# Kernel optimization log

Hardware: AMD Instinct MI355X
Metric: run time of the kernel (lower is better)

Reference implementation:

```python
import jax, jax.numpy as jnp
import numpy as np

N = 50000
E = 1600000
F_IN = 4
F_OUT = 32
PERIODS = 12


def setup_inputs() -> dict:
    key = jax.random.key(0)
    ks = jax.random.split(key, 18)
    s_in = 1.0 / np.sqrt(F_IN)
    s_cat = 1.0 / np.sqrt(2 * F_OUT)
    s_out = 1.0 / np.sqrt(F_OUT)
    inp = {
        'x': jax.random.normal(ks[0], (N, F_IN, PERIODS), dtype=jnp.float32),
        'edge_index': jax.random.randint(ks[1], (2, E), 0, N, dtype=jnp.int32),
        'attention': jax.random.uniform(ks[2], (PERIODS,), dtype=jnp.float32),
        # GRU update gate z: GCNConv weight/bias + Linear(2*F_OUT -> F_OUT)
        'Wz': jax.random.normal(ks[3], (F_IN, F_OUT), jnp.float32) * s_in,
        'bz': jnp.zeros((F_OUT,), jnp.float32),
        'Lz': jax.random.normal(ks[4], (2 * F_OUT, F_OUT), jnp.float32) * s_cat,
        'lz': jnp.zeros((F_OUT,), jnp.float32),
        # reset gate r
        'Wr': jax.random.normal(ks[5], (F_IN, F_OUT), jnp.float32) * s_in,
        'br': jnp.zeros((F_OUT,), jnp.float32),
        'Lr': jax.random.normal(ks[6], (2 * F_OUT, F_OUT), jnp.float32) * s_cat,
        'lr': jnp.zeros((F_OUT,), jnp.float32),
        # candidate h
        'Wh': jax.random.normal(ks[7], (F_IN, F_OUT), jnp.float32) * s_in,
        'bh': jnp.zeros((F_OUT,), jnp.float32),
        'Lh': jax.random.normal(ks[8], (2 * F_OUT, F_OUT), jnp.float32) * s_cat,
        'lh': jnp.zeros((F_OUT,), jnp.float32),
        # outer Linear(32 -> periods)
        'Wo': jax.random.normal(ks[9], (F_OUT, PERIODS), jnp.float32) * s_out,
        'bo': jnp.zeros((PERIODS,), jnp.float32),
    }
    return inp


def reference(x, edge_index, attention, Wz, bz, Lz, lz, Wr, br, Lr, lr, Wh, bh, Lh, lh, Wo, bo):
    n = x.shape[0]
    # gcn_norm: add self loops, symmetric D^-1/2 (A+I) D^-1/2
    loop = jnp.arange(n, dtype=edge_index.dtype)
    row = jnp.concatenate([edge_index[0], loop])  # source
    col = jnp.concatenate([edge_index[1], loop])  # target
    w = jnp.ones(row.shape[0], dtype=x.dtype)
    deg = jax.ops.segment_sum(w, col, num_segments=n)
    dinv = jnp.where(deg > 0, jax.lax.rsqrt(deg), 0.0)
    norm = dinv[row] * dinv[col]  # [E+N]

    def conv(xt, W, b):
        h = xt @ W                                   # [N, F_OUT]
        msg = h[row] * norm[:, None]                 # gather + scale
        return jax.ops.segment_sum(msg, col, num_segments=n) + b

    H0 = jnp.zeros((n, F_OUT), dtype=x.dtype)  # A3TGCN passes H=None each period

    def tgcn(xt):
        Z = jax.nn.sigmoid(jnp.concatenate([conv(xt, Wz, bz), H0], axis=1) @ Lz + lz)
        R = jax.nn.sigmoid(jnp.concatenate([conv(xt, Wr, br), H0], axis=1) @ Lr + lr)
        Ht = jnp.tanh(jnp.concatenate([conv(xt, Wh, bh), H0 * R], axis=1) @ Lh + lh)
        return Z * H0 + (1.0 - Z) * Ht

    Hs = jax.vmap(tgcn)(jnp.moveaxis(x, 2, 0))       # [T, N, F_OUT]
    probs = jax.nn.softmax(attention)
    H = jnp.einsum('tnc,t->nc', Hs, probs)           # attention-weighted sum over periods
    return jax.nn.relu(H) @ Wo + bo                  # [N, PERIODS]
```

## Files before the change

kernel.cpp:

```cpp
#include <hip/hip_runtime.h>
#include <hip/hip_fp16.h>
#include <math.h>

#define CHUNK 4096
#define CAPG  5120
#define GNODES 21

union U2H { uint2 u; __half2 h[2]; };

__global__ void k_pre(const float* __restrict__ Wz, const float* __restrict__ Lz, const float* __restrict__ lz,
                      const float* __restrict__ Wh, const float* __restrict__ Lh, const float* __restrict__ lh,
                      const float* __restrict__ bz, const float* __restrict__ bh,
                      const float* __restrict__ att,
                      float* __restrict__ AzT, float* __restrict__ AhT,
                      float* __restrict__ bzp, float* __restrict__ bhp, float* __restrict__ probs,
                      int* __restrict__ gcur) {
  int t = threadIdx.x;
  gcur[t] = 0;
  if (t < 128) {
    int f = t >> 2, k = t & 3;
    float s = 0.f, s2 = 0.f;
    for (int j = 0; j < 32; ++j) {
      s  = fmaf(Wz[k * 32 + j], Lz[j * 32 + f], s);
      s2 = fmaf(Wh[k * 32 + j], Lh[j * 32 + f], s2);
    }
    AzT[t] = s; AhT[t] = s2;
  }
  if (t >= 128 && t < 160) {
    int f = t - 128;
    float s = lz[f], s2 = lh[f];
    for (int j = 0; j < 32; ++j) {
      s  = fmaf(bz[j], Lz[j * 32 + f], s);
      s2 = fmaf(bh[j], Lh[j * 32 + f], s2);
    }
    bzp[f] = s; bhp[f] = s2;
  }
  if (t == 160) {
    float m = att[0];
    for (int i = 1; i < 12; ++i) m = fmaxf(m, att[i]);
    float e[12]; float s = 0.f;
    for (int i = 0; i < 12; ++i) { e[i] = __expf(att[i] - m); s += e[i]; }
    for (int i = 0; i < 12; ++i) probs[i] = e[i] / s;
  }
}

__global__ __launch_bounds__(512) void k_part(const int* __restrict__ row, const int* __restrict__ col,
                                              int E, int nbkt,
                                              int* __restrict__ gcur, unsigned* __restrict__ part) {
  __shared__ unsigned spak[CHUNK];
  __shared__ unsigned short sboth[CHUNK];
  __shared__ int hist[512], sscan[512], scur[512], gbase[512];
  int t = threadIdx.x;
  int base = blockIdx.x * CHUNK;
  int cnt = E - base; if (cnt > CHUNK) cnt = CHUNK;
  hist[t] = 0;
  __syncthreads();
  for (int i = t; i < cnt; i += 512) {
    int c = col[base + i];
    sboth[i] = (unsigned short)c;
    atomicAdd(&hist[c >> 7], 1);
  }
  __syncthreads();
  int v = hist[t];
  sscan[t] = v;
  __syncthreads();
  for (int off = 1; off < 512; off <<= 1) {
    int a = (t >= off) ? sscan[t - off] : 0;
    __syncthreads();
    sscan[t] += a;
    __syncthreads();
  }
  int excl = sscan[t] - v;
  gbase[t] = (v > 0) ? atomicAdd(&gcur[t], v) : 0;
  scur[t] = 0;
  __syncthreads();
  sscan[t] = excl;
  __syncthreads();
  for (int i = t; i < cnt; i += 512) {
    int c = (int)sboth[i];
    int b = c >> 7;
    int pos = atomicAdd(&scur[b], 1);
    spak[sscan[b] + pos] = ((unsigned)row[base + i] << 7) | (unsigned)(c & 127);
  }
  __syncthreads();
  int wave = t >> 6, lane = t & 63;
  for (int b = wave; b < nbkt; b += 8) {
    int len = hist[b], gb = gbase[b], src = sscan[b];
    int lim = CAPG - gb; if (lim > len) lim = len;
    unsigned* dst = part + (size_t)b * CAPG + gb;
    for (int j = lane; j < lim; j += 64) dst[j] = spak[src + j];
  }
}

__global__ __launch_bounds__(512) void k_sort(const unsigned* __restrict__ part, const int* __restrict__ gcur,
                                              const float4* __restrict__ x4,
                                              int* __restrict__ csr, int2* __restrict__ rng,
                                              float* __restrict__ dinv, uint2* __restrict__ xh2, int n) {
  __shared__ unsigned sedge[CAPG];
  __shared__ int hist[128], soff[128], scur2[128];
  __shared__ float sdi[128];
  int b = blockIdx.x, t = threadIdx.x;
  int cnt = gcur[b]; if (cnt > CAPG) cnt = CAPG;
  const unsigned* src = part + (size_t)b * CAPG;
  if (t < 128) hist[t] = 0;
  __syncthreads();
  for (int i = t; i < cnt; i += 512) {
    unsigned e = src[i];
    sedge[i] = e;
    atomicAdd(&hist[e & 127u], 1);
  }
  __syncthreads();
  int v = 0;
  if (t < 128) { v = hist[t]; soff[t] = v; }
  __syncthreads();
  for (int off = 1; off < 128; off <<= 1) {
    int a = 0;
    if (t < 128 && t >= off) a = soff[t - off];
    __syncthreads();
    if (t < 128) soff[t] += a;
    __syncthreads();
  }
  int base = b * CAPG;
  if (t < 128) {
    int excl = soff[t] - v;
    int node = b * 128 + t;
    float di = rsqrtf((float)(v + 1));
    sdi[t] = di;
    if (node < n) {
      rng[node] = make_int2(base + excl, base + excl + v);
      dinv[node] = di;
    }
    soff[t] = excl;
    scur2[t] = 0;
  }
  __syncthreads();
  for (int i = t; i < cnt; i += 512) {
    unsigned e = sedge[i];
    int lc = (int)(e & 127u);
    int pos = atomicAdd(&scur2[lc], 1);
    csr[base + soff[lc] + pos] = (int)(e >> 7);
  }
  int gb = b * 1536;
  for (int j = t; j < 1536; j += 512) {
    int gi = gb + j;
    if (gi < n * 12) {
      float4 f = x4[gi];
      float d = sdi[j / 12];
      __half2 h0 = __floats2half2_rn(d * f.x, d * f.y);
      __half2 h1 = __floats2half2_rn(d * f.z, d * f.w);
      uint2 u; u.x = *(unsigned*)&h0; u.y = *(unsigned*)&h1;
      xh2[gi] = u;
    }
  }
}

__global__ __launch_bounds__(256) void k_gather(const int* __restrict__ csr, const int2* __restrict__ rng,
                                                const float* __restrict__ dinv, const uint2* __restrict__ xh2,
                                                float4* __restrict__ Y4, int n) {
  int t = threadIdx.x;
  int grp = t / 12, c = t - grp * 12;
  if (grp >= GNODES) return;
  int node = blockIdx.x * GNODES + grp;
  if (node >= n) return;
  U2H s; s.u = xh2[(size_t)node * 12 + c];
  float2 f0 = __half22float2(s.h[0]), f1 = __half22float2(s.h[1]);
  float a0 = f0.x, a1 = f0.y, a2 = f1.x, a3 = f1.y;
  int2 r = rng[node];
  int e = r.x, end = r.y;
#define ACC4(V) { \
    float2 g0 = __half22float2(V.h[0]), g1 = __half22float2(V.h[1]); \
    a0 += g0.x; a1 += g0.y; a2 += g1.x; a3 += g1.y; }
  for (; e + 8 <= end; e += 8) {
    int r0 = csr[e],     r1 = csr[e + 1], r2 = csr[e + 2], r3 = csr[e + 3];
    int r4 = csr[e + 4], r5 = csr[e + 5], r6 = csr[e + 6], r7 = csr[e + 7];
    U2H v0, v1, v2, v3, v4, v5, v6, v7;
    v0.u = xh2[(size_t)r0 * 12 + c];
    v1.u = xh2[(size_t)r1 * 12 + c];
    v2.u = xh2[(size_t)r2 * 12 + c];
    v3.u = xh2[(size_t)r3 * 12 + c];
    v4.u = xh2[(size_t)r4 * 12 + c];
    v5.u = xh2[(size_t)r5 * 12 + c];
    v6.u = xh2[(size_t)r6 * 12 + c];
    v7.u = xh2[(size_t)r7 * 12 + c];
    ACC4(v0) ACC4(v1) ACC4(v2) ACC4(v3) ACC4(v4) ACC4(v5) ACC4(v6) ACC4(v7)
  }
  for (; e < end; ++e) {
    int r0 = csr[e];
    U2H v0; v0.u = xh2[(size_t)r0 * 12 + c];
    ACC4(v0)
  }
#undef ACC4
  float di = dinv[node];
  Y4[(size_t)node * 12 + c] = make_float4(a0 * di, a1 * di, a2 * di, a3 * di);
}

__global__ __launch_bounds__(256) void k_dense(
    const float4* __restrict__ Y4,
    const float* __restrict__ AzT, const float* __restrict__ AhT,
    const float* __restrict__ bzp, const float* __restrict__ bhp,
    const float* __restrict__ probs,
    const float* __restrict__ Wo, const float* __restrict__ bo,
    float* __restrict__ out, int n) {
  __shared__ float4 sAz4[32], sAh4[32];
  __shared__ float sbzp[32], sbhp[32], sprobs[12], sbo[12];
  __shared__ float sWo[384];
  __shared__ float4 sY4[96];
  __shared__ float sH[8 * 33];

  int t = threadIdx.x;
  int nb = blockIdx.x * 8;

  if (t < 32) {
    sAz4[t] = ((const float4*)AzT)[t];
    sAh4[t] = ((const float4*)AhT)[t];
    sbzp[t] = bzp[t];
    sbhp[t] = bhp[t];
  }
  if (t >= 32 && t < 44) { sprobs[t - 32] = probs[t - 32]; sbo[t - 32] = bo[t - 32]; }
  for (int i = t; i < 384; i += 256) sWo[i] = Wo[i];
  if (t < 96) {
    int gi = nb * 12 + t;
    if (gi < n * 12) sY4[t] = Y4[gi];
  }
  __syncthreads();

  int ln = t >> 5, f = t & 31;
  float4 az = sAz4[f], ah = sAh4[f];
  float bzf = sbzp[f], bhf = sbhp[f];
  const float* y = (const float*)sY4 + ln * 48;
  float Hf = 0.f;
#pragma unroll
  for (int tt = 0; tt < 12; ++tt) {
    float y0 = y[tt], y1 = y[12 + tt], y2 = y[24 + tt], y3 = y[36 + tt];
    float za = fmaf(az.x, y0, fmaf(az.y, y1, fmaf(az.z, y2, fmaf(az.w, y3, bzf))));
    float ha = fmaf(ah.x, y0, fmaf(ah.y, y1, fmaf(ah.z, y2, fmaf(ah.w, y3, bhf))));
    float ez = __expf(za);
    float ax = fabsf(ha);
    float e2 = __expf(-2.f * ax);
    float g = (1.f - e2) / ((1.f + ez) * (1.f + e2));
    Hf = fmaf(sprobs[tt], copysignf(g, ha), Hf);
  }
  sH[ln * 33 + f] = fmaxf(Hf, 0.f);
  __syncthreads();

  if (t < 96) {
    int ln2 = t / 12, p = t - ln2 * 12;
    int node2 = nb + ln2;
    if (node2 < n) {
      float acc = sbo[p];
      const float* h = &sH[ln2 * 33];
      const float* wv = &sWo[p];
#pragma unroll
      for (int f2 = 0; f2 < 32; ++f2) acc = fmaf(h[f2], wv[f2 * 12], acc);
      out[node2 * 12 + p] = acc;
    }
  }
}

extern "C" void kernel_launch(void* const* d_in, const int* in_sizes, int n_in,
                              void* d_out, int out_size, void* d_ws, size_t ws_size,
                              hipStream_t stream) {
  const float* x   = (const float*)d_in[0];
  const int*   ei  = (const int*)d_in[1];
  const float* att = (const float*)d_in[2];
  const float* Wz  = (const float*)d_in[3];
  const float* bz  = (const float*)d_in[4];
  const float* Lz  = (const float*)d_in[5];
  const float* lz  = (const float*)d_in[6];
  const float* Wh  = (const float*)d_in[11];
  const float* bh  = (const float*)d_in[12];
  const float* Lh  = (const float*)d_in[13];
  const float* lh  = (const float*)d_in[14];
  const float* Wo  = (const float*)d_in[15];
  const float* bo  = (const float*)d_in[16];
  float* out = (float*)d_out;

  const int N = in_sizes[0] / (4 * 12);
  const int E = in_sizes[1] / 2;
  const int NBKT = (N + 127) >> 7;
  const int* row = ei;
  const int* col = ei + E;

  char* w = (char*)d_ws;
  size_t o = 0;
  auto alloc = [&](size_t bytes) -> char* {
    o = (o + 255) & ~(size_t)255;
    char* p = w + o; o += bytes; return p;
  };
  float* pAzT   = (float*)alloc(128 * 4);
  float* pAhT   = (float*)alloc(128 * 4);
  float* pbzp   = (float*)alloc(32 * 4);
  float* pbhp   = (float*)alloc(32 * 4);
  float* pprobs = (float*)alloc(12 * 4);
  int*   pgcur  = (int*)alloc(512 * 4);
  float* pdinv  = (float*)alloc((size_t)NBKT * 128 * 4);
  int2*  prng   = (int2*)alloc((size_t)N * 8);
  unsigned* ppart = (unsigned*)alloc((size_t)NBKT * CAPG * 4);
  int*   pcsr   = (int*)alloc((size_t)NBKT * CAPG * 4);
  uint2* pxh    = (uint2*)alloc((size_t)NBKT * 128 * 12 * 8);
  float* pY     = (float*)alloc((size_t)N * 48 * 4);
  (void)ws_size; (void)n_in; (void)out_size;

  k_pre<<<1, 512, 0, stream>>>(Wz, Lz, lz, Wh, Lh, lh, bz, bh, att,
                               pAzT, pAhT, pbzp, pbhp, pprobs, pgcur);
  k_part<<<(E + CHUNK - 1) / CHUNK, 512, 0, stream>>>(row, col, E, NBKT, pgcur, ppart);
  k_sort<<<NBKT, 512, 0, stream>>>(ppart, pgcur, (const float4*)x, pcsr, prng, pdinv, pxh, N);
  k_gather<<<(N + GNODES - 1) / GNODES, 256, 0, stream>>>(pcsr, prng, pdinv, pxh,
                                                          (float4*)pY, N);
  k_dense<<<(N + 7) / 8, 256, 0, stream>>>((const float4*)pY, pAzT, pAhT, pbzp, pbhp, pprobs,
                                           Wo, bo, out, N);
}
```

Measured before the change: 186.4 us.

## Fuse gather with dense gating, flat partition scatter, prescale CSR indices

Merges the neighbour-aggregation kernel and the dense GRU/attention/output kernel into one, keeping the aggregated features in shared memory so the intermediate Y buffer is no longer written to and read back from global memory. The partition kernel now scatters edges with a flat per-element loop tagged with a bucket id, replacing the per-wave per-bucket copy, and uses a smaller chunk size. CSR entries are stored premultiplied by 12 to drop an index multiply in the gather, and gcur is zeroed with a memset instead of inside k_pre. The fused kernel repeats the weight loads into shared memory in every block and uses more shared memory per block, which may reduce occupancy during the latency-bound gather.

```diff
diff --git a/kernel.cpp b/kernel.cpp
--- a/kernel.cpp
+++ b/kernel.cpp
@@ -2,7 +2,7 @@
 #include <hip/hip_fp16.h>
 #include <math.h>
 
-#define CHUNK 4096
+#define CHUNK 2048
 #define CAPG  5120
 #define GNODES 21
 
@@ -13,10 +13,8 @@
                       const float* __restrict__ bz, const float* __restrict__ bh,
                       const float* __restrict__ att,
                       float* __restrict__ AzT, float* __restrict__ AhT,
-                      float* __restrict__ bzp, float* __restrict__ bhp, float* __restrict__ probs,
-                      int* __restrict__ gcur) {
+                      float* __restrict__ bzp, float* __restrict__ bhp, float* __restrict__ probs) {
   int t = threadIdx.x;
-  gcur[t] = 0;
   if (t < 128) {
     int f = t >> 2, k = t & 3;
     float s = 0.f, s2 = 0.f;
@@ -49,6 +47,7 @@
                                               int* __restrict__ gcur, unsigned* __restrict__ part) {
   __shared__ unsigned spak[CHUNK];
   __shared__ unsigned short sboth[CHUNK];
+  __shared__ unsigned short sdst[CHUNK];
   __shared__ int hist[512], sscan[512], scur[512], gbase[512];
   int t = threadIdx.x;
   int base = blockIdx.x * CHUNK;
@@ -80,15 +79,15 @@
     int c = (int)sboth[i];
     int b = c >> 7;
     int pos = atomicAdd(&scur[b], 1);
-    spak[sscan[b] + pos] = ((unsigned)row[base + i] << 7) | (unsigned)(c & 127);
-  }
-  __syncthreads();
-  int wave = t >> 6, lane = t & 63;
-  for (int b = wave; b < nbkt; b += 8) {
-    int len = hist[b], gb = gbase[b], src = sscan[b];
-    int lim = CAPG - gb; if (lim > len) lim = len;
-    unsigned* dst = part + (size_t)b * CAPG + gb;
-    for (int j = lane; j < lim; j += 64) dst[j] = spak[src + j];
+    int j = sscan[b] + pos;
+    spak[j] = ((unsigned)row[base + i] << 7) | (unsigned)(c & 127);
+    sdst[j] = (unsigned short)b;
+  }
+  __syncthreads();
+  for (int i = t; i < cnt; i += 512) {
+    int b = (int)sdst[i];
+    int gb = gbase[b] + (i - sscan[b]);
+    if (gb < CAPG) part[(size_t)b * CAPG + gb] = spak[i];
   }
 }
 
@@ -138,7 +137,7 @@
     unsigned e = sedge[i];
     int lc = (int)(e & 127u);
     int pos = atomicAdd(&scur2[lc], 1);
-    csr[base + soff[lc] + pos] = (int)(e >> 7);
+    csr[base + soff[lc] + pos] = (int)(e >> 7) * 12;
   }
   int gb = b * 1536;
   for (int j = t; j < 1536; j += 512) {
@@ -156,100 +155,87 @@
 
 __global__ __launch_bounds__(256) void k_gather(const int* __restrict__ csr, const int2* __restrict__ rng,
                                                 const float* __restrict__ dinv, const uint2* __restrict__ xh2,
-                                                float4* __restrict__ Y4, int n) {
+                                                const float* __restrict__ AzT, const float* __restrict__ AhT,
+                                                const float* __restrict__ bzp, const float* __restrict__ bhp,
+                                                const float* __restrict__ probs,
+                                                const float* __restrict__ Wo, const float* __restrict__ bo,
+                                                float* __restrict__ out, int n) {
+  __shared__ float sY[GNODES * 49];
+  __shared__ float sH[GNODES * 33];
+  __shared__ float4 sAz4[32], sAh4[32];
+  __shared__ float sbzp[32], sbhp[32], sprobs[12], sbo[12], sWo[384];
   int t = threadIdx.x;
+  int nb = blockIdx.x * GNODES;
+
+  if (t < 32) {
+    sAz4[t] = ((const float4*)AzT)[t];
+    sAh4[t] = ((const float4*)AhT)[t];
+    sbzp[t] = bzp[t]; sbhp[t] = bhp[t];
+  }
+  if (t >= 32 && t < 44) { sprobs[t - 32] = probs[t - 32]; sbo[t - 32] = bo[t - 32]; }
+  for (int i = t; i < 384; i += 256) sWo[i] = Wo[i];
+
   int grp = t / 12, c = t - grp * 12;
-  if (grp >= GNODES) return;
-  int node = blockIdx.x * GNODES + grp;
-  if (node >= n) return;
-  U2H s; s.u = xh2[(size_t)node * 12 + c];
-  float2 f0 = __half22float2(s.h[0]), f1 = __half22float2(s.h[1]);
-  float a0 = f0.x, a1 = f0.y, a2 = f1.x, a3 = f1.y;
-  int2 r = rng[node];
-  int e = r.x, end = r.y;
+  int node = nb + grp;
+  if (grp < GNODES && node < n) {
+    const uint2* xb = xh2 + c;
+    U2H s; s.u = xb[(size_t)node * 12];
+    float2 f0 = __half22float2(s.h[0]), f1 = __half22float2(s.h[1]);
+    float a0 = f0.x, a1 = f0.y, a2 = f1.x, a3 = f1.y;
+    int2 r = rng[node];
+    int e = r.x, end = r.y;
 #define ACC4(V) { \
     float2 g0 = __half22float2(V.h[0]), g1 = __half22float2(V.h[1]); \
     a0 += g0.x; a1 += g0.y; a2 += g1.x; a3 += g1.y; }
-  for (; e + 8 <= end; e += 8) {
-    int r0 = csr[e],     r1 = csr[e + 1], r2 = csr[e + 2], r3 = csr[e + 3];
-    int r4 = csr[e + 4], r5 = csr[e + 5], r6 = csr[e + 6], r7 = csr[e + 7];
-    U2H v0, v1, v2, v3, v4, v5, v6, v7;
-    v0.u = xh2[(size_t)r0 * 12 + c];
-    v1.u = xh2[(size_t)r1 * 12 + c];
-    v2.u = xh2[(size_t)r2 * 12 + c];
-    v3.u = xh2[(size_t)r3 * 12 + c];
-    v4.u = xh2[(size_t)r4 * 12 + c];
-    v5.u = xh2[(size_t)r5 * 12 + c];
-    v6.u = xh2[(size_t)r6 * 12 + c];
-    v7.u = xh2[(size_t)r7 * 12 + c];
-    ACC4(v0) ACC4(v1) ACC4(v2) ACC4(v3) ACC4(v4) ACC4(v5) ACC4(v6) ACC4(v7)
-  }
-  for (; e < end; ++e) {
-    int r0 = csr[e];
-    U2H v0; v0.u = xh2[(size_t)r0 * 12 + c];
-    ACC4(v0)
-  }
+    for (; e + 8 <= end; e += 8) {
+      int r0 = csr[e],     r1 = csr[e + 1], r2 = csr[e + 2], r3 = csr[e + 3];
+      int r4 = csr[e + 4], r5 = csr[e + 5], r6 = csr[e + 6], r7 = csr[e + 7];
+      U2H v0, v1, v2, v3, v4, v5, v6, v7;
+      v0.u = xb[r0]; v1.u = xb[r1]; v2.u = xb[r2]; v3.u = xb[r3];
+      v4.u = xb[r4]; v5.u = xb[r5]; v6.u = xb[r6]; v7.u = xb[r7];
+      ACC4(v0) ACC4(v1) ACC4(v2) ACC4(v3) ACC4(v4) ACC4(v5) ACC4(v6) ACC4(v7)
+    }
+    for (; e < end; ++e) {
+      int r0 = csr[e];
+      U2H v0; v0.u = xb[r0];
+      ACC4(v0)
+    }
 #undef ACC4
-  float di = dinv[node];
-  Y4[(size_t)node * 12 + c] = make_float4(a0 * di, a1 * di, a2 * di, a3 * di);
-}
-
-__global__ __launch_bounds__(256) void k_dense(
-    const float4* __restrict__ Y4,
-    const float* __restrict__ AzT, const float* __restrict__ AhT,
-    const float* __restrict__ bzp, const float* __restrict__ bhp,
-    const float* __restrict__ probs,
-    const float* __restrict__ Wo, const float* __restrict__ bo,
-    float* __restrict__ out, int n) {
-  __shared__ float4 sAz4[32], sAh4[32];
-  __shared__ float sbzp[32], sbhp[32], sprobs[12], sbo[12];
-  __shared__ float sWo[384];
-  __shared__ float4 sY4[96];
-  __shared__ float sH[8 * 33];
-
-  int t = threadIdx.x;
-  int nb = blockIdx.x * 8;
-
-  if (t < 32) {
-    sAz4[t] = ((const float4*)AzT)[t];
-    sAh4[t] = ((const float4*)AhT)[t];
-    sbzp[t] = bzp[t];
-    sbhp[t] = bhp[t];
-  }
-  if (t >= 32 && t < 44) { sprobs[t - 32] = probs[t - 32]; sbo[t - 32] = bo[t - 32]; }
-  for (int i = t; i < 384; i += 256) sWo[i] = Wo[i];
-  if (t < 96) {
-    int gi = nb * 12 + t;
-    if (gi < n * 12) sY4[t] = Y4[gi];
-  }
-  __syncthreads();
-
-  int ln = t >> 5, f = t & 31;
-  float4 az = sAz4[f], ah = sAh4[f];
-  float bzf = sbzp[f], bhf = sbhp[f];
-  const float* y = (const float*)sY4 + ln * 48;
-  float Hf = 0.f;
+    float di = dinv[node];
+    float* yb = sY + grp * 49 + c * 4;
+    yb[0] = a0 * di; yb[1] = a1 * di; yb[2] = a2 * di; yb[3] = a3 * di;
+  }
+  __syncthreads();
+
+  for (int u = t; u < GNODES * 32; u += 256) {
+    int ln = u >> 5, f = u & 31;
+    if (nb + ln >= n) continue;
+    const float* y = sY + ln * 49;
+    float4 az = sAz4[f], ah = sAh4[f];
+    float bzf = sbzp[f], bhf = sbhp[f];
+    float acc = 0.f;
 #pragma unroll
-  for (int tt = 0; tt < 12; ++tt) {
-    float y0 = y[tt], y1 = y[12 + tt], y2 = y[24 + tt], y3 = y[36 + tt];
-    float za = fmaf(az.x, y0, fmaf(az.y, y1, fmaf(az.z, y2, fmaf(az.w, y3, bzf))));
-    float ha = fmaf(ah.x, y0, fmaf(ah.y, y1, fmaf(ah.z, y2, fmaf(ah.w, y3, bhf))));
-    float ez = __expf(za);
-    float ax = fabsf(ha);
-    float e2 = __expf(-2.f * ax);
-    float g = (1.f - e2) / ((1.f + ez) * (1.f + e2));
-    Hf = fmaf(sprobs[tt], copysignf(g, ha), Hf);
-  }
-  sH[ln * 33 + f] = fmaxf(Hf, 0.f);
-  __syncthreads();
-
-  if (t < 96) {
-    int ln2 = t / 12, p = t - ln2 * 12;
-    int node2 = nb + ln2;
+    for (int tt = 0; tt < 12; ++tt) {
+      float y0 = y[tt], y1 = y[12 + tt], y2 = y[24 + tt], y3 = y[36 + tt];
+      float za = fmaf(az.x, y0, fmaf(az.y, y1, fmaf(az.z, y2, fmaf(az.w, y3, bzf))));
+      float ha = fmaf(ah.x, y0, fmaf(ah.y, y1, fmaf(ah.z, y2, fmaf(ah.w, y3, bhf))));
+      float ez = __expf(za);
+      float ax = fabsf(ha);
+      float e2 = __expf(-2.f * ax);
+      float g = (1.f - e2) / ((1.f + ez) * (1.f + e2));
+      acc = fmaf(sprobs[tt], copysignf(g, ha), acc);
+    }
+    sH[ln * 33 + f] = fmaxf(acc, 0.f);
+  }
+  __syncthreads();
+
+  if (t < GNODES * 12) {
+    int ln = t / 12, p = t - ln * 12;
+    int node2 = nb + ln;
     if (node2 < n) {
       float acc = sbo[p];
-      const float* h = &sH[ln2 * 33];
-      const float* wv = &sWo[p];
+      const float* h = sH + ln * 33;
+      const float* wv = sWo + p;
 #pragma unroll
       for (int f2 = 0; f2 < 32; ++f2) acc = fmaf(h[f2], wv[f2 * 12], acc);
       out[node2 * 12 + p] = acc;
@@ -298,15 +284,14 @@
   unsigned* ppart = (unsigned*)alloc((size_t)NBKT * CAPG * 4);
   int*   pcsr   = (int*)alloc((size_t)NBKT * CAPG * 4);
   uint2* pxh    = (uint2*)alloc((size_t)NBKT * 128 * 12 * 8);
-  float* pY     = (float*)alloc((size_t)N * 48 * 4);
   (void)ws_size; (void)n_in; (void)out_size;
 
-  k_pre<<<1, 512, 0, stream>>>(Wz, Lz, lz, Wh, Lh, lh, bz, bh, att,
-                               pAzT, pAhT, pbzp, pbhp, pprobs, pgcur);
+  hipMemsetAsync(pgcur, 0, 512 * 4, stream);
+  k_pre<<<1, 256, 0, stream>>>(Wz, Lz, lz, Wh, Lh, lh, bz, bh, att,
+                               pAzT, pAhT, pbzp, pbhp, pprobs);
   k_part<<<(E + CHUNK - 1) / CHUNK, 512, 0, stream>>>(row, col, E, NBKT, pgcur, ppart);
   k_sort<<<NBKT, 512, 0, stream>>>(ppart, pgcur, (const float4*)x, pcsr, prng, pdinv, pxh, N);
   k_gather<<<(N + GNODES - 1) / GNODES, 256, 0, stream>>>(pcsr, prng, pdinv, pxh,
-                                                          (float4*)pY, N);
-  k_dense<<<(N + 7) / 8, 256, 0, stream>>>((const float4*)pY, pAzT, pAhT, pbzp, pbhp, pprobs,
-                                           Wo, bo, out, N);
-}
+                                                          pAzT, pAhT, pbzp, pbhp, pprobs,
+                                                          Wo, bo, out, N);
+}
```

After: 180.3 us. 1.03x faster.
